# Optimization experiments

Hardware: AMD Instinct MI355X
Metric: run time of the kernel (lower is better)

Reference implementation:

```python
import jax, jax.numpy as jnp
import numpy as np

B, T, C, H = 4, 2048, 1024, 16
DH = C // H


def setup_inputs() -> dict:
    key = jax.random.key(0)
    k1, k2, k3 = jax.random.split(key, 3)
    x = jax.random.normal(k1, (B, T, C), dtype=jnp.float32)
    w_attn = jax.random.normal(k2, (C, 3 * C), dtype=jnp.float32) * 0.02
    w_proj = jax.random.normal(k3, (C, C), dtype=jnp.float32) * 0.02
    return {"x": x, "w_attn": w_attn, "w_proj": w_proj}


def reference(x, w_attn, w_proj):
    b, t, c = x.shape
    qkv = x @ w_attn  # [B,T,3C]
    q, k, v = jnp.split(qkv, 3, axis=2)
    # [B,T,C] -> [B,H,T,DH]
    q = q.reshape(b, t, H, DH).transpose(0, 2, 1, 3)
    k = k.reshape(b, t, H, DH).transpose(0, 2, 1, 3)
    v = v.reshape(b, t, H, DH).transpose(0, 2, 1, 3)
    scale = 1.0 / np.sqrt(DH).astype(np.float32)
    att = jnp.einsum('bhqd,bhkd->bhqk', q, k) * scale  # [B,H,T,T]
    causal = jnp.tril(jnp.ones((t, t), dtype=bool))
    att = jnp.where(causal[None, None], att, jnp.finfo(att.dtype).min)
    att = jax.nn.softmax(att, axis=-1)
    y = jnp.einsum('bhqk,bhkd->bhqd', att, v)  # [B,H,T,DH]
    y = y.transpose(0, 2, 1, 3).reshape(b, t, c)
    return y @ w_proj
```

## Files before the change

kernel.cpp:

```cpp
#include <hip/hip_runtime.h>
#include <hip/hip_bf16.h>

typedef unsigned short u16;
typedef __attribute__((ext_vector_type(8))) __bf16 bf16x8;
typedef __attribute__((ext_vector_type(4))) float f32x4;
typedef u16 u16x8 __attribute__((ext_vector_type(8)));
typedef u16x8 u16x8a __attribute__((may_alias));
typedef f32x4 f32x4a __attribute__((may_alias));

constexpr int Bz = 4, T = 2048, Cdim = 1024, H = 16, DH = 64;
constexpr int Mrows = Bz * T;
constexpr int N_QKV = 3 * Cdim;
constexpr int Kdim = Cdim;
constexpr float C1 = 0.18033688011118324f;
constexpr float C2 = 34.62468098133512f;

__device__ __forceinline__ u16 f2bf(float f) {
    union { float f; unsigned u; } x; x.f = f;
    if ((x.u & 0x7f800000u) == 0x7f800000u) return 0;
    unsigned r = x.u + 0x7fffu + ((x.u >> 16) & 1u);
    return (u16)(r >> 16);
}

__device__ __forceinline__ bf16x8 as_bf(u16x8 v) {
    union { u16x8 u; bf16x8 b; } x; x.u = v; return x.b;
}

__global__ __launch_bounds__(256) void transpose_cvt(
    const float* __restrict__ W, u16* __restrict__ WT, int K, int N)
{
    const int n = blockIdx.x * 256 + threadIdx.x;
    const int k8 = blockIdx.y * 8;
    u16x8 p;
#pragma unroll
    for (int i = 0; i < 8; ++i) p[i] = f2bf(W[(long)(k8 + i) * N + n]);
    *(u16x8a*)&WT[(long)n * K + k8] = p;
}

template <int MODE>
__global__ __launch_bounds__(256) void gemm_kernel(
    const void* __restrict__ Av, const u16* __restrict__ Bw,
    float* __restrict__ out,
    u16* __restrict__ qb, u16* __restrict__ kb, u16* __restrict__ vtb,
    int Nsz, int Ksz)
{
    constexpr int BM = 128, BN = 128, BK = 32;
    constexpr int AS = 40, BS = 40;
    __shared__ __align__(16) u16 As[BM * AS];
    __shared__ __align__(16) u16 Bt[BN * BS];

    const float* Af = (const float*)Av;
    const u16*   Ab = (const u16*)Av;

    const int tid = threadIdx.x;
    const int w = tid >> 6, lane = tid & 63, quad = lane >> 4, lr = lane & 15;
    const int wr = (w >> 1) * 64, wc = (w & 1) * 64;
    const int m0 = blockIdx.y * BM, n0 = blockIdx.x * BN;

    f32x4 acc[4][4] = {};

    for (int k0 = 0; k0 < Ksz; k0 += BK) {
#pragma unroll
        for (int s = 0; s < 2; ++s) {
            int v = tid + s * 256;
            int row = v >> 2, c8 = (v & 3) * 8;
            if (MODE == 1) {
                const float* src = &Af[(long)(m0 + row) * Ksz + k0 + c8];
                f32x4 a0 = *(const f32x4a*)src;
                f32x4 a1 = *(const f32x4a*)(src + 4);
                u16x8 p;
                p[0] = f2bf(a0[0]); p[1] = f2bf(a0[1]); p[2] = f2bf(a0[2]); p[3] = f2bf(a0[3]);
                p[4] = f2bf(a1[0]); p[5] = f2bf(a1[1]); p[6] = f2bf(a1[2]); p[7] = f2bf(a1[3]);
                *(u16x8a*)&As[row * AS + c8] = p;
            } else {
                int m = m0 + row, c = k0 + c8;
                int b = m >> 11, t = m & (T - 1), h = c >> 6, d = c & 63;
                long src = (((long)(b * H + h)) * T + t) * DH + d;
                *(u16x8a*)&As[row * AS + c8] = *(const u16x8a*)&Ab[src];
            }
        }
#pragma unroll
        for (int s = 0; s < 2; ++s) {
            int v = tid + s * 256;
            int row = v >> 2, c8 = (v & 3) * 8;
            *(u16x8a*)&Bt[row * BS + c8] =
                *(const u16x8a*)&Bw[(long)(n0 + row) * Ksz + k0 + c8];
        }
        __syncthreads();

        bf16x8 af[4];
#pragma unroll
        for (int it = 0; it < 4; ++it)
            af[it] = as_bf(*(const u16x8a*)&As[(wr + it * 16 + lr) * AS + quad * 8]);
#pragma unroll
        for (int jt = 0; jt < 4; ++jt) {
            bf16x8 bfv = as_bf(*(const u16x8a*)&Bt[(wc + jt * 16 + lr) * BS + quad * 8]);
#pragma unroll
            for (int it = 0; it < 4; ++it)
                acc[it][jt] = __builtin_amdgcn_mfma_f32_16x16x32_bf16(af[it], bfv, acc[it][jt], 0, 0, 0);
        }
        __syncthreads();
    }

#pragma unroll
    for (int it = 0; it < 4; ++it) {
#pragma unroll
        for (int jt = 0; jt < 4; ++jt) {
#pragma unroll
            for (int r = 0; r < 4; ++r) {
                int m = m0 + wr + it * 16 + quad * 4 + r;
                int n = n0 + wc + jt * 16 + lr;
                if (MODE == 2) {
                    out[(long)m * Nsz + n] = acc[it][jt][r];
                } else {
                    u16 hv = f2bf(acc[it][jt][r]);
                    int b = m >> 11, t = m & (T - 1);
                    int sec = n >> 10, rem = n & 1023, h = rem >> 6, d = rem & 63;
                    int bh = b * H + h;
                    if (sec == 0)      qb [((long)bh * T + t) * DH + d] = hv;
                    else if (sec == 1) kb [((long)bh * T + t) * DH + d] = hv;
                    else               vtb[((long)bh * DH + d) * T + t] = hv;
                }
            }
        }
    }
}

__global__ __launch_bounds__(256) void attn_kernel(
    const u16* qbuf, const u16* __restrict__ kbuf,
    const u16* __restrict__ vtbuf, u16* yb)
{
    constexpr int KS = 72;
    constexpr int PS = 68;
    __shared__ __align__(16) u16 Ks[64 * KS];
    __shared__ __align__(16) u16 Vts[64 * KS];
    __shared__ __align__(16) float Psf[128 * PS];

    const int tid = threadIdx.x;
    const int w = tid >> 6, lane = tid & 63, quad = lane >> 4, lr = lane & 15;
    const int pairi = blockIdx.x;
    const int bh = blockIdx.y;

    const u16* qbase  = qbuf  + (long)bh * T * DH;
    const u16* kbase  = kbuf  + (long)bh * T * DH;
    const u16* vtbase = vtbuf + (long)bh * DH * T;
    u16* ybase = yb + (long)bh * T * DH;

    const int sr0 = tid >> 3;
    const int sc0 = (tid & 7) * 8;

    u16x8 ones_u;
#pragma unroll
    for (int i = 0; i < 8; ++i) ones_u[i] = 0x3F80;
    const bf16x8 onesf = as_bf(ones_u);

    for (int qsel = 0; qsel < 2; ++qsel) {
        const int qblk = qsel ? (15 - pairi) : pairi;
        const int q0 = qblk * 128;

        bf16x8 qf[2][2];
#pragma unroll
        for (int mt = 0; mt < 2; ++mt)
#pragma unroll
            for (int st = 0; st < 2; ++st)
                qf[mt][st] = as_bf(*(const u16x8a*)
                    &qbase[(q0 + w * 32 + mt * 16 + lr) * DH + quad * 8 + st * 32]);

        f32x4 o[2][4] = {};
        f32x4 accl[2] = {};

        const int ktmax = 2 * qblk + 1;

        u16x8 kreg[2], vreg[2];
#pragma unroll
        for (int s = 0; s < 2; ++s) {
            int row = sr0 + s * 32;
            kreg[s] = *(const u16x8a*)&kbase[(long)row * DH + sc0];
            vreg[s] = *(const u16x8a*)&vtbase[(long)row * T + sc0];
        }

        for (int kt = 0; kt <= ktmax; ++kt) {
#pragma unroll
            for (int s = 0; s < 2; ++s) {
                int row = sr0 + s * 32;
                *(u16x8a*)&Ks[row * KS + sc0]  = kreg[s];
                *(u16x8a*)&Vts[row * KS + sc0] = vreg[s];
            }
            __syncthreads();

            if (kt < ktmax) {
#pragma unroll
                for (int s = 0; s < 2; ++s) {
                    int row = sr0 + s * 32;
                    kreg[s] = *(const u16x8a*)&kbase[(long)((kt + 1) * 64 + row) * DH + sc0];
                    vreg[s] = *(const u16x8a*)&vtbase[(long)row * T + (kt + 1) * 64 + sc0];
                }
            }

            f32x4 s_acc[2][4] = {};
#pragma unroll
            for (int st = 0; st < 2; ++st) {
#pragma unroll
                for (int nt = 0; nt < 4; ++nt) {
                    bf16x8 kf = as_bf(*(const u16x8a*)&Ks[(nt * 16 + lr) * KS + quad * 8 + st * 32]);
#pragma unroll
                    for (int mt = 0; mt < 2; ++mt)
                        s_acc[mt][nt] = __builtin_amdgcn_mfma_f32_16x16x32_bf16(
                            qf[mt][st], kf, s_acc[mt][nt], 0, 0, 0);
                }
            }

            if (kt >= 2 * qblk) {
#pragma unroll
                for (int mt = 0; mt < 2; ++mt)
#pragma unroll
                    for (int r = 0; r < 4; ++r) {
                        const int qrow = q0 + w * 32 + mt * 16 + quad * 4 + r;
                        const int prow = (w * 32 + mt * 16 + quad * 4 + r) * PS;
#pragma unroll
                        for (int nt = 0; nt < 4; ++nt) {
                            int key = kt * 64 + nt * 16 + lr;
                            float pv = (key <= qrow)
                                ? __builtin_exp2f(__builtin_fmaf(s_acc[mt][nt][r], C1, -C2))
                                : 0.f;
                            Psf[prow + nt * 16 + lr] = pv;
                        }
                    }
            } else {
#pragma unroll
                for (int mt = 0; mt < 2; ++mt)
#pragma unroll
                    for (int r = 0; r < 4; ++r) {
                        const int prow = (w * 32 + mt * 16 + quad * 4 + r) * PS;
#pragma unroll
                        for (int nt = 0; nt < 4; ++nt)
                            Psf[prow + nt * 16 + lr] =
                                __builtin_exp2f(__builtin_fmaf(s_acc[mt][nt][r], C1, -C2));
                    }
            }
            asm volatile("s_waitcnt lgkmcnt(0)" ::: "memory");

#pragma unroll
            for (int st = 0; st < 2; ++st) {
                bf16x8 pf[2];
#pragma unroll
                for (int mt = 0; mt < 2; ++mt) {
                    const float* pr = &Psf[(w * 32 + mt * 16 + lr) * PS + quad * 8 + st * 32];
                    f32x4 lo = *(const f32x4a*)pr;
                    f32x4 hi = *(const f32x4a*)(pr + 4);
                    union { u16x8 u; unsigned w32[4]; } pk;
                    asm("v_cvt_pk_bf16_f32 %0, %1, %2" : "=v"(pk.w32[0]) : "v"(lo[0]), "v"(lo[1]));
                    asm("v_cvt_pk_bf16_f32 %0, %1, %2" : "=v"(pk.w32[1]) : "v"(lo[2]), "v"(lo[3]));
                    asm("v_cvt_pk_bf16_f32 %0, %1, %2" : "=v"(pk.w32[2]) : "v"(hi[0]), "v"(hi[1]));
                    asm("v_cvt_pk_bf16_f32 %0, %1, %2" : "=v"(pk.w32[3]) : "v"(hi[2]), "v"(hi[3]));
                    pf[mt] = as_bf(pk.u);
                }
#pragma unroll
                for (int mt = 0; mt < 2; ++mt)
                    accl[mt] = __builtin_amdgcn_mfma_f32_16x16x32_bf16(
                        pf[mt], onesf, accl[mt], 0, 0, 0);
#pragma unroll
                for (int dt = 0; dt < 4; ++dt) {
                    bf16x8 vf = as_bf(*(const u16x8a*)&Vts[(dt * 16 + lr) * KS + quad * 8 + st * 32]);
#pragma unroll
                    for (int mt = 0; mt < 2; ++mt)
                        o[mt][dt] = __builtin_amdgcn_mfma_f32_16x16x32_bf16(
                            pf[mt], vf, o[mt][dt], 0, 0, 0);
                }
            }
            __syncthreads();
        }

#pragma unroll
        for (int mt = 0; mt < 2; ++mt) {
#pragma unroll
            for (int dt = 0; dt < 4; ++dt) {
#pragma unroll
                for (int r = 0; r < 4; ++r) {
                    int t = q0 + w * 32 + mt * 16 + quad * 4 + r;
                    int d = dt * 16 + lr;
                    float l = accl[mt][r];
                    float yv = (l > 1e-37f) ? o[mt][dt][r] / l : 0.f;
                    ybase[(long)t * DH + d] = f2bf(yv);
                }
            }
        }
    }
}

extern "C" void kernel_launch(void* const* d_in, const int* in_sizes, int n_in,
                              void* d_out, int out_size, void* d_ws, size_t ws_size,
                              hipStream_t stream) {
    const float* x      = (const float*)d_in[0];
    const float* w_attn = (const float*)d_in[1];
    const float* w_proj = (const float*)d_in[2];
    float* out = (float*)d_out;

    const size_t per = (size_t)Bz * H * T * DH;
    u16* qb  = (u16*)d_ws;
    u16* kb  = qb + per;
    u16* vtb = kb + per;

    u16* watT   = (u16*)d_out;
    u16* wprojT = kb;

    dim3 blk(256);
    transpose_cvt<<<dim3(N_QKV / 256, Kdim / 8), blk, 0, stream>>>(
        w_attn, watT, Kdim, N_QKV);
    gemm_kernel<1><<<dim3(N_QKV / 128, Mrows / 128), blk, 0, stream>>>(
        (const void*)x, watT, nullptr, qb, kb, vtb, N_QKV, Kdim);
    attn_kernel<<<dim3(8, Bz * H), blk, 0, stream>>>(qb, kb, vtb, qb);
    transpose_cvt<<<dim3(Cdim / 256, Kdim / 8), blk, 0, stream>>>(
        w_proj, wprojT, Kdim, Cdim);
    gemm_kernel<2><<<dim3(Cdim / 128, Mrows / 128), blk, 0, stream>>>(
        (const void*)qb, wprojT, out, nullptr, nullptr, nullptr, Cdim, Kdim);
}
```

Measured before the change: 321.3 us.

## Pre-convert x to bf16 and load GEMM tiles via direct global-to-LDS loads

Adds a separate kernel that converts x to bf16 into the output buffer, so the QKV GEMM reads bf16 input instead of converting fp32 inside the tile loader. Both GEMMs now fill shared memory with global_load_lds 16-byte direct loads, which bypass registers. BK grows to 64 and the padded shared-memory strides are dropped. The unpadded layout may cause LDS bank conflicts on fragment reads, and the extra conversion pass adds a full read and write of x.

```diff
diff --git a/kernel.cpp b/kernel.cpp
--- a/kernel.cpp
+++ b/kernel.cpp
@@ -26,6 +26,25 @@
     union { u16x8 u; bf16x8 b; } x; x.u = v; return x.b;
 }
 
+__device__ __forceinline__ void gload_lds16(const u16* g, u16* l) {
+    __builtin_amdgcn_global_load_lds(
+        (const __attribute__((address_space(1))) void*)g,
+        (__attribute__((address_space(3))) void*)l, 16, 0, 0);
+}
+
+__global__ __launch_bounds__(256) void cvt_x(
+    const float* __restrict__ X, u16* __restrict__ Xb, long n8)
+{
+    for (long i = blockIdx.x * 256 + threadIdx.x; i < n8; i += (long)gridDim.x * 256) {
+        f32x4 a0 = *(const f32x4a*)&X[i * 8];
+        f32x4 a1 = *(const f32x4a*)&X[i * 8 + 4];
+        u16x8 p;
+        p[0] = f2bf(a0[0]); p[1] = f2bf(a0[1]); p[2] = f2bf(a0[2]); p[3] = f2bf(a0[3]);
+        p[4] = f2bf(a1[0]); p[5] = f2bf(a1[1]); p[6] = f2bf(a1[2]); p[7] = f2bf(a1[3]);
+        *(u16x8a*)&Xb[i * 8] = p;
+    }
+}
+
 __global__ __launch_bounds__(256) void transpose_cvt(
     const float* __restrict__ W, u16* __restrict__ WT, int K, int N)
 {
@@ -39,65 +58,55 @@
 
 template <int MODE>
 __global__ __launch_bounds__(256) void gemm_kernel(
-    const void* __restrict__ Av, const u16* __restrict__ Bw,
+    const u16* __restrict__ Ab, const u16* __restrict__ Bw,
     float* __restrict__ out,
     u16* __restrict__ qb, u16* __restrict__ kb, u16* __restrict__ vtb,
     int Nsz, int Ksz)
 {
-    constexpr int BM = 128, BN = 128, BK = 32;
-    constexpr int AS = 40, BS = 40;
-    __shared__ __align__(16) u16 As[BM * AS];
-    __shared__ __align__(16) u16 Bt[BN * BS];
-
-    const float* Af = (const float*)Av;
-    const u16*   Ab = (const u16*)Av;
+    constexpr int BM = 128, BN = 128, BK = 64;
+    __shared__ __align__(16) u16 As[BM * BK];
+    __shared__ __align__(16) u16 Bt[BN * BK];
 
     const int tid = threadIdx.x;
     const int w = tid >> 6, lane = tid & 63, quad = lane >> 4, lr = lane & 15;
     const int wr = (w >> 1) * 64, wc = (w & 1) * 64;
     const int m0 = blockIdx.y * BM, n0 = blockIdx.x * BN;
 
+    const int lrow = lane >> 3;
+    const int lcol = (lane & 7) * 8;
+
     f32x4 acc[4][4] = {};
 
     for (int k0 = 0; k0 < Ksz; k0 += BK) {
 #pragma unroll
-        for (int s = 0; s < 2; ++s) {
-            int v = tid + s * 256;
-            int row = v >> 2, c8 = (v & 3) * 8;
+        for (int s = 0; s < 4; ++s) {
+            const int chunk = w * 4 + s;
+            const int r = chunk * 8 + lrow;
+            const u16* asrc;
             if (MODE == 1) {
-                const float* src = &Af[(long)(m0 + row) * Ksz + k0 + c8];
-                f32x4 a0 = *(const f32x4a*)src;
-                f32x4 a1 = *(const f32x4a*)(src + 4);
-                u16x8 p;
-                p[0] = f2bf(a0[0]); p[1] = f2bf(a0[1]); p[2] = f2bf(a0[2]); p[3] = f2bf(a0[3]);
-                p[4] = f2bf(a1[0]); p[5] = f2bf(a1[1]); p[6] = f2bf(a1[2]); p[7] = f2bf(a1[3]);
-                *(u16x8a*)&As[row * AS + c8] = p;
+                asrc = &Ab[(long)(m0 + r) * Ksz + k0 + lcol];
             } else {
-                int m = m0 + row, c = k0 + c8;
-                int b = m >> 11, t = m & (T - 1), h = c >> 6, d = c & 63;
-                long src = (((long)(b * H + h)) * T + t) * DH + d;
-                *(u16x8a*)&As[row * AS + c8] = *(const u16x8a*)&Ab[src];
-            }
-        }
-#pragma unroll
-        for (int s = 0; s < 2; ++s) {
-            int v = tid + s * 256;
-            int row = v >> 2, c8 = (v & 3) * 8;
-            *(u16x8a*)&Bt[row * BS + c8] =
-                *(const u16x8a*)&Bw[(long)(n0 + row) * Ksz + k0 + c8];
+                const int m = m0 + r, b = m >> 11, t = m & (T - 1), h = k0 >> 6;
+                asrc = &Ab[(((long)(b * H + h)) * T + t) * DH + lcol];
+            }
+            gload_lds16(asrc, &As[chunk * 512]);
+            gload_lds16(&Bw[(long)(n0 + r) * Ksz + k0 + lcol], &Bt[chunk * 512]);
         }
         __syncthreads();
 
-        bf16x8 af[4];
-#pragma unroll
-        for (int it = 0; it < 4; ++it)
-            af[it] = as_bf(*(const u16x8a*)&As[(wr + it * 16 + lr) * AS + quad * 8]);
-#pragma unroll
-        for (int jt = 0; jt < 4; ++jt) {
-            bf16x8 bfv = as_bf(*(const u16x8a*)&Bt[(wc + jt * 16 + lr) * BS + quad * 8]);
+#pragma unroll
+        for (int ks = 0; ks < 2; ++ks) {
+            bf16x8 af[4];
 #pragma unroll
             for (int it = 0; it < 4; ++it)
-                acc[it][jt] = __builtin_amdgcn_mfma_f32_16x16x32_bf16(af[it], bfv, acc[it][jt], 0, 0, 0);
+                af[it] = as_bf(*(const u16x8a*)&As[(wr + it * 16 + lr) * BK + ks * 32 + quad * 8]);
+#pragma unroll
+            for (int jt = 0; jt < 4; ++jt) {
+                bf16x8 bfv = as_bf(*(const u16x8a*)&Bt[(wc + jt * 16 + lr) * BK + ks * 32 + quad * 8]);
+#pragma unroll
+                for (int it = 0; it < 4; ++it)
+                    acc[it][jt] = __builtin_amdgcn_mfma_f32_16x16x32_bf16(af[it], bfv, acc[it][jt], 0, 0, 0);
+            }
         }
         __syncthreads();
     }
@@ -301,17 +310,19 @@
     u16* kb  = qb + per;
     u16* vtb = kb + per;
 
-    u16* watT   = (u16*)d_out;
+    u16* xb     = (u16*)d_out;
+    u16* watT   = xb + (size_t)Mrows * Kdim;
     u16* wprojT = kb;
 
     dim3 blk(256);
+    cvt_x<<<dim3(2048), blk, 0, stream>>>(x, xb, (long)Mrows * Kdim / 8);
     transpose_cvt<<<dim3(N_QKV / 256, Kdim / 8), blk, 0, stream>>>(
         w_attn, watT, Kdim, N_QKV);
     gemm_kernel<1><<<dim3(N_QKV / 128, Mrows / 128), blk, 0, stream>>>(
-        (const void*)x, watT, nullptr, qb, kb, vtb, N_QKV, Kdim);
+        xb, watT, nullptr, qb, kb, vtb, N_QKV, Kdim);
     attn_kernel<<<dim3(8, Bz * H), blk, 0, stream>>>(qb, kb, vtb, qb);
     transpose_cvt<<<dim3(Cdim / 256, Kdim / 8), blk, 0, stream>>>(
         w_proj, wprojT, Kdim, Cdim);
     gemm_kernel<2><<<dim3(Cdim / 128, Mrows / 128), blk, 0, stream>>>(
-        (const void*)qb, wprojT, out, nullptr, nullptr, nullptr, Cdim, Kdim);
-}
+        qb, wprojT, out, nullptr, nullptr, nullptr, Cdim, Kdim);
+}
```

Result: faster. 292.8 us (-8.9%).
